# Kernel optimization log

Measured on AMD Instinct MI355X. Metric: run time of the kernel, lower is better.

The kernel has to match this reference:

```python
import jax, jax.numpy as jnp
import numpy as np

C = 16          # number of classes
LAM = 25.0      # lambda_param (invariance)
MU = 25.0       # mu_param (variance)
NU = 1.0        # nu_param (covariance)
ALPHA = 50.0    # alpha_param (class-discriminative margin & weight)
EPS = 1e-4


def setup_inputs() -> dict:
    key = jax.random.key(0)
    k1, k2, k3 = jax.random.split(key, 3)
    N, D = 32768, 256
    z_a = jax.random.normal(k1, (N, D), dtype=jnp.float32)
    z_b = jax.random.normal(k2, (N, D), dtype=jnp.float32)
    labels = jax.random.randint(k3, (N,), 0, C)
    return {"z_a": z_a, "z_b": z_b, "labels": labels}


def _class_stats(x, labels):
    # counts [C], mean [C,D], unbiased var [C,D] via one segmented pass
    ones = jnp.ones(x.shape[0], x.dtype)
    counts = jax.ops.segment_sum(ones, labels, num_segments=C)
    s = jax.ops.segment_sum(x, labels, num_segments=C)
    sq = jax.ops.segment_sum(x * x, labels, num_segments=C)
    mean = s / counts[:, None]
    var = (sq - counts[:, None] * mean * mean) / (counts[:, None] - 1.0)
    return counts, mean, var


def _variance_loss(var):
    # mean over classes of mean_D relu(1 - std); D equal per class -> global mean
    std = jnp.sqrt(var + EPS)
    return jnp.mean(jax.nn.relu(1.0 - std))


def _covariance_loss(x, labels, counts, mean):
    D = x.shape[1]
    e = x - mean[labels]  # centered per class

    def per_class(c):
        w = (labels == c).astype(x.dtype)
        em = e * w[:, None]
        cov = em.T @ em / (counts[c] - 1.0)  # [D, D]
        off = (cov * cov).sum() - (jnp.diagonal(cov) ** 2).sum()
        return off / D

    return jnp.mean(jax.lax.map(per_class, jnp.arange(C)))


def _class_disc_loss(mean_a, mean_b):
    m = 0.5 * (mean_a + mean_b)               # [C, D]
    diff = m[:, None, :] - m[None, :, :]      # [C, C, D]
    d2 = jnp.sum(diff * diff, axis=-1)        # [C, C]
    mask = jnp.triu(jnp.ones((C, C), bool), 1)
    dist = jnp.sqrt(jnp.where(mask, d2, 1.0))  # safe sqrt off-mask
    pen = jnp.where(mask, jax.nn.relu(ALPHA - dist) ** 2, 0.0)
    npairs = C * (C - 1) // 2
    return pen.sum() / npairs


def reference(z_a, z_b, labels):
    inv_loss = jnp.mean((z_a - z_b) ** 2)
    ca, ma, va = _class_stats(z_a, labels)
    cb, mb, vb = _class_stats(z_b, labels)
    var_loss = 0.5 * (_variance_loss(va) + _variance_loss(vb))
    cov_loss = 0.5 * (_covariance_loss(z_a, labels, ca, ma)
                      + _covariance_loss(z_b, labels, cb, mb))
    class_loss = _class_disc_loss(ma, mb)
    return LAM * inv_loss + MU * var_loss + NU * cov_loss + ALPHA * class_loss
```

## Files before the change

kernel.cpp:

```cpp
#include <hip/hip_runtime.h>
#include <math.h>

#define N_ROWS 32768
#define D 256
#define C 16

#define WS_SUMS_A 0
#define WS_SQ_A   4096
#define WS_SUMS_B 8192
#define WS_SQ_B   12288
#define WS_INV    16384
#define WS_COV    16385
#define WS_COUNTS 16392
#define WS_CURSOR 16408
#define WS_POFFP  16424
#define WS_EOFF   16448
#define WS_INVP   16512
#define WS_COVP   17024
#define WS_PERM   17920
#define WS_ZERO_FLOATS 16408

#define WS_PSUM   50688
#define WS_HPART  181760
#define WS_GPART2 189952
#define GP_TILE2P 2048
#define NTASK     10
#define NSPLIT    8
#define KC        2
#define GP_PER_SPLIT2P (NTASK * C * 2 * GP_TILE2P)
#define RIDX_CAP  1024
#define NEED_A ((size_t)(WS_GPART2 + NSPLIT * GP_PER_SPLIT2P) * 4)

typedef __attribute__((ext_vector_type(8))) __bf16 bf16x8;
typedef __attribute__((ext_vector_type(16))) float f32x16;

__device__ inline unsigned bf16_rne(float f) {
    unsigned u = __float_as_uint(f);
    return (u + 0x7fffu + ((u >> 16) & 1u)) >> 16;
}
__device__ inline unsigned pack_bf16(float lo, float hi) {
    return bf16_rne(lo) | (bf16_rne(hi) << 16);
}
__device__ inline int img_base4(int c, int kd) {
    return c * 20 + ((kd + ((c >> 1) & 12)) & 12);
}
__device__ inline int img_base2(int c, int kd) {
    return c * 20 + ((kd + ((c >> 1) & 12)) & 14);
}
__device__ inline void task_rc(int w, int& r, int& c) {
    if (w < 4)      { r = 0; c = w; }
    else if (w < 7) { r = 1; c = w - 3; }
    else if (w < 9) { r = 2; c = w - 5; }
    else            { r = 3; c = 3; }
}


__global__ __launch_bounds__(256) void k_pre(const float* __restrict__ za,
                                             const float* __restrict__ zb,
                                             const int* __restrict__ labels,
                                             int* __restrict__ hpart,
                                             float* __restrict__ ws) {
    const int t = threadIdx.x;
    const int b = blockIdx.x;
    __shared__ int h[C];
    if (t < C) h[t] = 0;
    __syncthreads();
    if (t < 64) atomicAdd(&h[labels[b * 64 + t]], 1);

    const int base = b * 4096 + t;
    float acc = 0.f;
    #pragma unroll
    for (int k = 0; k < 16; ++k) {
        const int i = base + k * 256;
        const float4 a = ((const float4*)za)[i];
        const float4 v = ((const float4*)zb)[i];
        const float dx = a.x - v.x, dy = a.y - v.y;
        const float dz = a.z - v.z, dw = a.w - v.w;
        acc += dx * dx + dy * dy + dz * dz + dw * dw;
    }
    for (int o = 32; o > 0; o >>= 1) acc += __shfl_down(acc, o, 64);
    __shared__ float red[4];
    if ((t & 63) == 0) red[t >> 6] = acc;
    __syncthreads();
    if (t < C) hpart[b * C + t] = h[t];
    if (t == 0) ws[WS_INVP + b] = red[0] + red[1] + red[2] + red[3];
}

__global__ __launch_bounds__(512) void k_scatter2(const int* __restrict__ labels,
                                                  const int* __restrict__ hpart,
                                                  int* __restrict__ counts,
                                                  int* __restrict__ poffp,
                                                  int* __restrict__ eoffp,
                                                  int* __restrict__ perm) {
    const int t = threadIdx.x;
    const int B = blockIdx.x;
    __shared__ int lh[C];
    __shared__ int tot[32][C];
    __shared__ int pre[32][C];
    __shared__ int ccnt[C], cpre[C], ceoff[C];
    const int i = B * 512 + t;
    const int lab = labels[i];
    if (t < C) lh[t] = 0;
    const int c = t & 15, seg = t >> 4;
    {
        int tt = 0, pp = 0;
        const int plo = seg * 16, pcut = B * 8;
        #pragma unroll
        for (int p = plo; p < plo + 16; ++p) {
            const int v = hpart[p * C + c];
            tt += v;
            if (p < pcut) pp += v;
        }
        tot[seg][c] = tt;
        pre[seg][c] = pp;
    }
    __syncthreads();
    const int lr = atomicAdd(&lh[lab], 1);
    if (t < C) {
        int s1 = 0, s2 = 0;
        #pragma unroll
        for (int g = 0; g < 32; ++g) { s1 += tot[g][t]; s2 += pre[g][t]; }
        ccnt[t] = s1;
        cpre[t] = s2;
    }
    __syncthreads();
    if (t == 0) {
        int off = 0, po = 0;
        for (int cc = 0; cc < C; ++cc) {
            ceoff[cc] = off;
            if (B == 0) { eoffp[cc] = off; poffp[cc] = po; counts[cc] = ccnt[cc]; }
            off += ccnt[cc];
            po += (ccnt[cc] + 31) >> 5;
        }
        if (B == 0) { eoffp[C] = off; poffp[C] = po; }
    }
    __syncthreads();
    perm[ceoff[lab] + cpre[lab] + lr] = i;
}

__global__ __launch_bounds__(640) void k_gram6(const float* __restrict__ za,
                                               const float* __restrict__ zb,
                                               const int* __restrict__ perm,
                                               const int* __restrict__ counts,
                                               const int* __restrict__ poffp,
                                               const int* __restrict__ eoffp,
                                               float* __restrict__ ws) {
    const int t = threadIdx.x;
    const int split = blockIdx.x;
    const int cls = blockIdx.y, inp = blockIdx.z;
    const float* X = inp ? zb : za;
    const int cnt = counts[cls];
    const int eoff = eoffp[cls];
    const int nsteps = poffp[cls + 1] - poffp[cls];
    const int chunk = (nsteps + NSPLIT - 1) / NSPLIT;
    const int sb = split * chunk;
    const int se = min(sb + chunk, nsteps);

    __shared__ __align__(16) unsigned img[2][5120];
    __shared__ float sstats[512];
    __shared__ int ridx[RIDX_CAP];

    for (int i = t; i < 512; i += 640) sstats[i] = 0.f;
    const int nl = (se > sb) ? (se - sb) * 32 : 0;
    for (int i = t; i < nl && i < RIDX_CAP; i += 640) {
        const int gr = sb * 32 + i;
        ridx[i] = (gr < cnt) ? perm[eoff + gr] : -1;
    }
    __syncthreads();

    auto rowidx = [&](int li) -> int {
        if (li < RIDX_CAP) return ridx[li];
        const int gr = sb * 32 + li;
        return (gr < cnt) ? perm[eoff + gr] : -1;
    };

    const int lane = t & 63, w = t >> 6;
    const int cg = lane & 31, q = lane >> 5;
    int tr, tc;
    task_rc(w, tr, tc);
    const bool stg = (t < 512);

    const int lc = 4 * (t & 63);
    const int kp0 = 2 * ((t >> 6) & 7);

    f32x16 acc[2][2];
    #pragma unroll
    for (int i = 0; i < 2; ++i)
        #pragma unroll
        for (int j = 0; j < 2; ++j) acc[i][j] = 0.0f;

    float s1r[4] = {0.f, 0.f, 0.f, 0.f};
    float s2r[4] = {0.f, 0.f, 0.f, 0.f};
    float4 f0[2], f1[2];

    auto load_regs = [&](int s) {
        #pragma unroll
        for (int it = 0; it < 2; ++it) {
            const int li = (s - sb) * 32 + 2 * (kp0 + it);
            const int r0 = rowidx(li), r1 = rowidx(li + 1);
            f0[it] = (r0 >= 0) ? *(const float4*)(X + (size_t)r0 * D + lc)
                               : make_float4(0.f, 0.f, 0.f, 0.f);
            f1[it] = (r1 >= 0) ? *(const float4*)(X + (size_t)r1 * D + lc)
                               : make_float4(0.f, 0.f, 0.f, 0.f);
        }
    };
    auto pack_store = [&](int buf) {
        unsigned pw[4][2];
        #pragma unroll
        for (int it = 0; it < 2; ++it) {
            pw[0][it] = pack_bf16(f0[it].x, f1[it].x);
            pw[1][it] = pack_bf16(f0[it].y, f1[it].y);
            pw[2][it] = pack_bf16(f0[it].z, f1[it].z);
            pw[3][it] = pack_bf16(f0[it].w, f1[it].w);
        }
        #pragma unroll
        for (int d = 0; d < 4; ++d)
            *(uint2*)&img[buf][img_base2(lc + d, kp0)] = make_uint2(pw[d][0], pw[d][1]);
        #pragma unroll
        for (int it = 0; it < 2; ++it) {
            s1r[0] += f0[it].x + f1[it].x; s2r[0] += f0[it].x * f0[it].x + f1[it].x * f1[it].x;
            s1r[1] += f0[it].y + f1[it].y; s2r[1] += f0[it].y * f0[it].y + f1[it].y * f1[it].y;
            s1r[2] += f0[it].z + f1[it].z; s2r[2] += f0[it].z * f0[it].z + f1[it].z * f1[it].z;
            s1r[3] += f0[it].w + f1[it].w; s2r[3] += f0[it].w * f0[it].w + f1[it].w * f1[it].w;
        }
    };
    auto frag = [&](int buf, int col, int kd) -> bf16x8 {
        return *(const bf16x8*)&img[buf][img_base4(col, kd)];
    };

    if (sb < se) {
        if (stg) { load_regs(sb); pack_store(0); }
        __syncthreads();
        for (int s = sb; s < se; ++s) {
            const int buf = (s - sb) & 1;
            const bool more = (s + 1 < se);
            if (stg && more) load_regs(s + 1);
            #pragma unroll
            for (int h = 0; h < 2; ++h) {
                const int kd = h * 8 + q * 4;
                bf16x8 a0 = frag(buf, tr * 64 + cg, kd);
                bf16x8 a1 = frag(buf, tr * 64 + 32 + cg, kd);
                bf16x8 b0, b1;
                if (tr == tc) { b0 = a0; b1 = a1; }
                else {
                    b0 = frag(buf, tc * 64 + cg, kd);
                    b1 = frag(buf, tc * 64 + 32 + cg, kd);
                }
                acc[0][0] = __builtin_amdgcn_mfma_f32_32x32x16_bf16(a0, b0, acc[0][0], 0, 0, 0);
                acc[0][1] = __builtin_amdgcn_mfma_f32_32x32x16_bf16(a0, b1, acc[0][1], 0, 0, 0);
                acc[1][0] = __builtin_amdgcn_mfma_f32_32x32x16_bf16(a1, b0, acc[1][0], 0, 0, 0);
                acc[1][1] = __builtin_amdgcn_mfma_f32_32x32x16_bf16(a1, b1, acc[1][1], 0, 0, 0);
            }
            if (stg && more) pack_store(buf ^ 1);
            __syncthreads();
        }
    }

    unsigned* gp = (unsigned*)ws + WS_GPART2 + (size_t)split * GP_PER_SPLIT2P
                 + (((size_t)cls * 2 + inp) * NTASK + w) * GP_TILE2P;
    #pragma unroll
    for (int i = 0; i < 2; ++i)
        #pragma unroll
        for (int r = 0; r < 16; ++r) {
            const int row = i * 32 + (r & 3) + 8 * (r >> 2) + 4 * q;
            gp[row * 32 + cg] = pack_bf16(acc[i][0][r], acc[i][1][r]);
        }

    if (stg) {
        #pragma unroll
        for (int d = 0; d < 4; ++d) {
            atomicAdd(&sstats[lc + d],       s1r[d]);
            atomicAdd(&sstats[256 + lc + d], s2r[d]);
        }
    }
    __syncthreads();
    const size_t pbase = (((size_t)split * C + cls) * 2 + inp) * 512;
    for (int i = t; i < 512; i += 640) ws[WS_PSUM + pbase + i] = sstats[i];
}

__global__ __launch_bounds__(256) void k_cov4(const int* __restrict__ counts,
                                              float* __restrict__ ws) {
    const int t = threadIdx.x;
    const int w = blockIdx.x / KC, k0 = blockIdx.x % KC;
    int tr, tc;
    task_rc(w, tr, tc);
    const int cls = blockIdx.y, inp = blockIdx.z;
    const int cnt = counts[cls];
    const float fc = (float)cnt;
    const float cinv = 1.f / fc, uinv = 1.f / (fc - 1.f);
    const float wgt = (tr == tc) ? 1.f : 2.f;
    __shared__ float Mr[64], Mc[64];
    if (t < 64) {
        float s = 0.f;
        #pragma unroll
        for (int sp = 0; sp < NSPLIT; ++sp)
            s += ws[WS_PSUM + (((size_t)sp * C + cls) * 2 + inp) * 512 + tr * 64 + t];
        Mr[t] = s * cinv;
    } else if (t < 128) {
        const int u = t - 64;
        float s = 0.f;
        #pragma unroll
        for (int sp = 0; sp < NSPLIT; ++sp)
            s += ws[WS_PSUM + (((size_t)sp * C + cls) * 2 + inp) * 512 + tc * 64 + u];
        Mc[u] = s * cinv;
    }
    if (w == 0 && k0 == 0) {
        float s1 = 0.f, s2 = 0.f;
        #pragma unroll
        for (int sp = 0; sp < NSPLIT; ++sp) {
            const size_t pb = WS_PSUM + (((size_t)sp * C + cls) * 2 + inp) * 512;
            s1 += ws[pb + t];
            s2 += ws[pb + 256 + t];
        }
        ws[(inp ? WS_SUMS_B : WS_SUMS_A) + cls * D + t] = s1;
        ws[(inp ? WS_SQ_B   : WS_SQ_A)   + cls * D + t] = s2;
    }
    __syncthreads();

    const int e0 = k0 * 1024 + t * 4;
    const unsigned* gp0 = (const unsigned*)ws + WS_GPART2
                        + (((size_t)cls * 2 + inp) * NTASK + w) * GP_TILE2P + e0;
    uint4 u4[NSPLIT];
    #pragma unroll
    for (int sp = 0; sp < NSPLIT; ++sp)
        u4[sp] = *(const uint4*)(gp0 + (size_t)sp * GP_PER_SPLIT2P);

    float glo[4] = {0.f, 0.f, 0.f, 0.f};
    float ghi[4] = {0.f, 0.f, 0.f, 0.f};
    #pragma unroll
    for (int sp = 0; sp < NSPLIT; ++sp) {
        const unsigned* uu = (const unsigned*)&u4[sp];
        #pragma unroll
        for (int j = 0; j < 4; ++j) {
            glo[j] += __uint_as_float(uu[j] << 16);
            ghi[j] += __uint_as_float(uu[j] & 0xffff0000u);
        }
    }
    const int row = e0 >> 5, c0 = e0 & 31;
    const float mr = Mr[row];
    float local = 0.f;
    #pragma unroll
    for (int j = 0; j < 4; ++j) {
        const float clo = (glo[j] - fc * mr * Mc[c0 + j]) * uinv;
        const float chi = (ghi[j] - fc * mr * Mc[c0 + j + 32]) * uinv;
        if (!(tr == tc && row == c0 + j))      local += wgt * clo * clo;
        if (!(tr == tc && row == c0 + j + 32)) local += wgt * chi * chi;
    }
    for (int o = 32; o > 0; o >>= 1) local += __shfl_down(local, o, 64);
    __shared__ float red[4];
    if ((t & 63) == 0) red[t >> 6] = local;
    __syncthreads();
    if (t == 0)
        ws[WS_COVP + (((size_t)inp * C + cls) * NTASK + w) * KC + k0] =
            red[0] + red[1] + red[2] + red[3];
}

__global__ __launch_bounds__(512) void k_hist(const int* __restrict__ labels,
                                              int* __restrict__ counts) {
    __shared__ int h[C];
    const int t = threadIdx.x;
    if (t < C) h[t] = 0;
    __syncthreads();
    const int i = blockIdx.x * 512 + t;
    atomicAdd(&h[labels[i]], 1);
    __syncthreads();
    if (t < C) atomicAdd(&counts[t], h[t]);
}

__global__ void k_scan(const int* __restrict__ counts, int* __restrict__ cursor,
                       int* __restrict__ poffp, int* __restrict__ eoffp) {
    if (threadIdx.x == 0) {
        int off = 0, po = 0;
        for (int c = 0; c < C; ++c) {
            cursor[c] = off;
            eoffp[c] = off;
            poffp[c] = po;
            off += counts[c];
            po += (counts[c] + 31) >> 5;
        }
        poffp[C] = po;
        eoffp[C] = off;
    }
}

__global__ __launch_bounds__(512) void k_scatter(const int* __restrict__ labels,
                                                 int* __restrict__ cursor,
                                                 int* __restrict__ perm) {
    __shared__ int lh[C];
    __shared__ int lbase[C];
    const int t = threadIdx.x;
    if (t < C) lh[t] = 0;
    __syncthreads();
    const int i = blockIdx.x * 512 + t;
    const int lab = labels[i];
    const int lr = atomicAdd(&lh[lab], 1);
    __syncthreads();
    if (t < C) lbase[t] = atomicAdd(&cursor[t], lh[t]);
    __syncthreads();
    perm[lbase[lab] + lr] = i;
}

__global__ __launch_bounds__(256) void k_stats(const float* __restrict__ za,
                                               const float* __restrict__ zb,
                                               const int* __restrict__ labels,
                                               float* __restrict__ ws) {
    const int t = threadIdx.x;
    __shared__ float S[4][C * D];
    __shared__ int lab[512];
    for (int i = t; i < 4 * C * D; i += 256) ((float*)S)[i] = 0.f;
    const int r0 = blockIdx.x * 512;
    for (int i = t; i < 512; i += 256) lab[i] = labels[r0 + i];
    __syncthreads();
    float invp = 0.f;
    #pragma unroll 4
    for (int rr = 0; rr < 512; ++rr) {
        const int l = lab[rr];
        const float a = za[(size_t)(r0 + rr) * D + t];
        const float b = zb[(size_t)(r0 + rr) * D + t];
        const float dd = a - b;
        invp += dd * dd;
        S[0][l * D + t] += a;
        S[1][l * D + t] += a * a;
        S[2][l * D + t] += b;
        S[3][l * D + t] += b * b;
    }
    __syncthreads();
    #pragma unroll
    for (int c = 0; c < C; ++c) {
        atomicAdd(&ws[WS_SUMS_A + c * D + t], S[0][c * D + t]);
        atomicAdd(&ws[WS_SQ_A   + c * D + t], S[1][c * D + t]);
        atomicAdd(&ws[WS_SUMS_B + c * D + t], S[2][c * D + t]);
        atomicAdd(&ws[WS_SQ_B   + c * D + t], S[3][c * D + t]);
    }
    for (int o = 32; o > 0; o >>= 1) invp += __shfl_down(invp, o, 64);
    if ((t & 63) == 0) atomicAdd(&ws[WS_INV], invp);
}

#define STR 20
#define KB 32
__global__ __launch_bounds__(256) void k_gram_slow(const float* __restrict__ za,
                                                   const float* __restrict__ zb,
                                                   const int* __restrict__ perm,
                                                   const int* __restrict__ counts,
                                                   float* __restrict__ ws) {
    const int t = threadIdx.x;
    const int tile = blockIdx.x;
    const int tx = tile >> 1, ty = (tile + 1) >> 1;
    const int cls = blockIdx.y;
    const int inp = blockIdx.z;
    const float* X = inp ? zb : za;
    const float* sums = ws + (inp ? WS_SUMS_B : WS_SUMS_A) + cls * D;
    int offs = 0;
    for (int c = 0; c < cls; ++c) offs += counts[c];
    const int cnt = counts[cls];
    const int cm0 = tx * 128, cn0 = ty * 128;
    __shared__ __align__(16) unsigned lds[2][256 * STR];
    const int p = t >> 5, cq = t & 31;
    const int lane = t & 63, w = t >> 6;
    const int wr = w & 1, wc = w >> 1;
    const int cg = lane & 31, q = lane >> 5;
    f32x16 acc[2][2];
    #pragma unroll
    for (int i = 0; i < 2; ++i)
        #pragma unroll
        for (int j = 0; j < 2; ++j) acc[i][j] = 0.0f;
    const int nsteps = (cnt + KB - 1) / KB;
    auto stage = [&](int buf, int k0) {
        #pragma unroll
        for (int ch = 0; ch < 2; ++ch) {
            const int gc = (ch ? cn0 : cm0) + 4 * cq;
            #pragma unroll
            for (int sub = 0; sub < 2; ++sub) {
                const int rr = sub * 16 + 2 * p;
                const int r0 = k0 + rr, r1 = r0 + 1;
                float4 v0 = make_float4(0.f, 0.f, 0.f, 0.f), v1 = v0;
                if (r0 < cnt) v0 = *(const float4*)(X + (size_t)perm[offs + r0] * D + gc);
                if (r1 < cnt) v1 = *(const float4*)(X + (size_t)perm[offs + r1] * D + gc);
                unsigned* dst = &lds[buf][(ch * 128 + 4 * cq) * STR + (rr >> 1)];
                dst[0 * STR] = pack_bf16(v0.x, v1.x);
                dst[1 * STR] = pack_bf16(v0.y, v1.y);
                dst[2 * STR] = pack_bf16(v0.z, v1.z);
                dst[3 * STR] = pack_bf16(v0.w, v1.w);
            }
        }
    };
    auto frag = [&](int buf, int colbase, int h) -> bf16x8 {
        return *(const bf16x8*)&lds[buf][(colbase + cg) * STR + h * 8 + q * 4];
    };
    stage(0, 0);
    for (int s = 0; s < nsteps; ++s) {
        __syncthreads();
        const int buf = s & 1;
        if (s + 1 < nsteps) stage(buf ^ 1, (s + 1) * KB);
        #pragma unroll
        for (int h = 0; h < 2; ++h) {
            bf16x8 a0 = frag(buf, wr * 64, h);
            bf16x8 a1 = frag(buf, wr * 64 + 32, h);
            bf16x8 b0 = frag(buf, 128 + wc * 64, h);
            bf16x8 b1 = frag(buf, 128 + wc * 64 + 32, h);
            acc[0][0] = __builtin_amdgcn_mfma_f32_32x32x16_bf16(a0, b0, acc[0][0], 0, 0, 0);
            acc[0][1] = __builtin_amdgcn_mfma_f32_32x32x16_bf16(a0, b1, acc[0][1], 0, 0, 0);
            acc[1][0] = __builtin_amdgcn_mfma_f32_32x32x16_bf16(a1, b0, acc[1][0], 0, 0, 0);
            acc[1][1] = __builtin_amdgcn_mfma_f32_32x32x16_bf16(a1, b1, acc[1][1], 0, 0, 0);
        }
    }
    const float fc = (float)cnt;
    const float cinv = 1.f / fc, uinv = 1.f / (fc - 1.f);
    const float wgt = (tx == ty) ? 1.f : 2.f;
    float local = 0.f;
    #pragma unroll
    for (int i = 0; i < 2; ++i) {
        #pragma unroll
        for (int j = 0; j < 2; ++j) {
            const int gn = cn0 + wc * 64 + j * 32 + (lane & 31);
            const float mn = sums[gn] * cinv;
            #pragma unroll
            for (int r = 0; r < 16; ++r) {
                const int row = (r & 3) + 8 * (r >> 2) + 4 * q;
                const int gm = cm0 + wr * 64 + i * 32 + row;
                const float cov = (acc[i][j][r] - fc * (sums[gm] * cinv) * mn) * uinv;
                if (gm != gn) local += wgt * cov * cov;
            }
        }
    }
    for (int o = 32; o > 0; o >>= 1) local += __shfl_down(local, o, 64);
    if (lane == 0) atomicAdd(&ws[WS_COV], local);
}

__global__ __launch_bounds__(256) void k_final(const float* __restrict__ ws,
                                               float* __restrict__ out,
                                               int fast) {
    __shared__ float M[C * D];
    __shared__ float redv[4], redi[4], redc[4], redp[4];
    const int t = threadIdx.x;
    const int* counts = (const int*)ws + WS_COUNTS;

    float vsum = 0.f;
    for (int idx = t; idx < 2 * C * D; idx += 256) {
        const int inp = idx >> 12;
        const int cd = idx & 4095;
        const int c = cd >> 8;
        const float cnt = (float)counts[c];
        const float s  = ws[(inp ? WS_SUMS_B : WS_SUMS_A) + cd];
        const float sq = ws[(inp ? WS_SQ_B   : WS_SQ_A)   + cd];
        const float mean = s / cnt;
        const float var = (sq - cnt * mean * mean) / (cnt - 1.f);
        vsum += fmaxf(1.f - sqrtf(var + 1e-4f), 0.f);
    }
    float isum, csum;
    if (fast) {
        isum = ws[WS_INVP + t] + ws[WS_INVP + 256 + t];
        csum = ws[WS_COVP + t] + ws[WS_COVP + 256 + t]
             + ((t < 128) ? ws[WS_COVP + 512 + t] : 0.f);
    } else {
        isum = (t == 0) ? ws[WS_INV] : 0.f;
        csum = (t == 0) ? ws[WS_COV] : 0.f;
    }
    for (int cd = t; cd < C * D; cd += 256) {
        const int c = cd >> 8;
        const float cnt = (float)counts[c];
        M[cd] = 0.5f * (ws[WS_SUMS_A + cd] + ws[WS_SUMS_B + cd]) / cnt;
    }
    for (int o = 32; o > 0; o >>= 1) {
        vsum += __shfl_down(vsum, o, 64);
        isum += __shfl_down(isum, o, 64);
        csum += __shfl_down(csum, o, 64);
    }
    if ((t & 63) == 0) {
        redv[t >> 6] = vsum; redi[t >> 6] = isum; redc[t >> 6] = csum;
    }
    __syncthreads();

    const int wv = t >> 6, ln = t & 63;
    float psum = 0.f;
    int p = 0;
    for (int i = 0; i < C; ++i) {
        for (int j = i + 1; j < C; ++j, ++p) {
            if ((p & 3) != wv) continue;
            float d2 = 0.f;
            #pragma unroll
            for (int d = ln; d < D; d += 64) {
                const float df = M[i * D + d] - M[j * D + d];
                d2 += df * df;
            }
            for (int o = 32; o > 0; o >>= 1) d2 += __shfl_down(d2, o, 64);
            if (ln == 0) {
                const float dist = sqrtf(d2);
                const float r = fmaxf(50.f - dist, 0.f);
                psum += r * r;
            }
        }
    }
    if (ln == 0) redp[wv] = psum;
    __syncthreads();

    if (t == 0) {
        const float var_loss = (redv[0] + redv[1] + redv[2] + redv[3]) / 8192.f;
        const float class_loss = (redp[0] + redp[1] + redp[2] + redp[3]) / 120.f;
        const float inv_loss = (redi[0] + redi[1] + redi[2] + redi[3]) / (float)(N_ROWS * D);
        const float cov_loss = 0.5f * (redc[0] + redc[1] + redc[2] + redc[3]) / (float)(C * D);
        out[0] = 25.f * inv_loss + 25.f * var_loss + 1.f * cov_loss + 50.f * class_loss;
    }
}

extern "C" void kernel_launch(void* const* d_in, const int* in_sizes, int n_in,
                              void* d_out, int out_size, void* d_ws, size_t ws_size,
                              hipStream_t stream) {
    const float* za = (const float*)d_in[0];
    const float* zb = (const float*)d_in[1];
    const int* labels = (const int*)d_in[2];
    float* out = (float*)d_out;
    float* ws = (float*)d_ws;
    int* wsi = (int*)d_ws;

    if (ws_size >= NEED_A) {
        k_pre<<<512, 256, 0, stream>>>(za, zb, labels, wsi + WS_HPART, ws);
        k_scatter2<<<64, 512, 0, stream>>>(labels, wsi + WS_HPART, wsi + WS_COUNTS,
                                           wsi + WS_POFFP, wsi + WS_EOFF, wsi + WS_PERM);
        k_gram6<<<dim3(NSPLIT, C, 2), 640, 0, stream>>>(
            za, zb, wsi + WS_PERM, wsi + WS_COUNTS, wsi + WS_POFFP,
            wsi + WS_EOFF, ws);
        k_cov4<<<dim3(NTASK * KC, C, 2), 256, 0, stream>>>(wsi + WS_COUNTS, ws);
        k_final<<<1, 256, 0, stream>>>(ws, out, 1);
    } else {
        hipMemsetAsync(d_ws, 0, WS_ZERO_FLOATS * sizeof(float), stream);
        k_hist<<<64, 512, 0, stream>>>(labels, wsi + WS_COUNTS);
        k_scan<<<1, 64, 0, stream>>>(wsi + WS_COUNTS, wsi + WS_CURSOR,
                                     wsi + WS_POFFP, wsi + WS_EOFF);
        k_scatter<<<64, 512, 0, stream>>>(labels, wsi + WS_CURSOR, wsi + WS_PERM);
        k_stats<<<64, 256, 0, stream>>>(za, zb, labels, ws);
        k_gram_slow<<<dim3(3, C, 2), 256, 0, stream>>>(za, zb, wsi + WS_PERM,
                                                       wsi + WS_COUNTS, ws);
        k_final<<<1, 256, 0, stream>>>(ws, out, 0);
    }
}
```

Baseline: 159.5 us.

## Fuse invariance loss into gram kernel and slim the histogram pre-pass

The separate pre-pass kernel read all of z_a and z_b only to compute the squared-difference sum. That work now happens inside the gram kernel: blocks for input A also load the matching z_b rows and accumulate the invariance term, writing one partial per split and class. The pre-pass shrinks to a label histogram over 64 blocks, and the scatter prefix logic is changed to match. This drops one full read of both inputs, but it doubles the global loads in the input-A gram blocks and so unbalances the work between inputs A and B.

```diff
diff --git a/kernel.cpp b/kernel.cpp
--- a/kernel.cpp
+++ b/kernel.cpp
@@ -55,35 +55,15 @@
 }
 
 
-__global__ __launch_bounds__(256) void k_pre(const float* __restrict__ za,
-                                             const float* __restrict__ zb,
-                                             const int* __restrict__ labels,
-                                             int* __restrict__ hpart,
-                                             float* __restrict__ ws) {
-    const int t = threadIdx.x;
-    const int b = blockIdx.x;
+__global__ __launch_bounds__(512) void k_hist2(const int* __restrict__ labels,
+                                               int* __restrict__ hpart) {
     __shared__ int h[C];
+    const int t = threadIdx.x;
     if (t < C) h[t] = 0;
     __syncthreads();
-    if (t < 64) atomicAdd(&h[labels[b * 64 + t]], 1);
-
-    const int base = b * 4096 + t;
-    float acc = 0.f;
-    #pragma unroll
-    for (int k = 0; k < 16; ++k) {
-        const int i = base + k * 256;
-        const float4 a = ((const float4*)za)[i];
-        const float4 v = ((const float4*)zb)[i];
-        const float dx = a.x - v.x, dy = a.y - v.y;
-        const float dz = a.z - v.z, dw = a.w - v.w;
-        acc += dx * dx + dy * dy + dz * dz + dw * dw;
-    }
-    for (int o = 32; o > 0; o >>= 1) acc += __shfl_down(acc, o, 64);
-    __shared__ float red[4];
-    if ((t & 63) == 0) red[t >> 6] = acc;
-    __syncthreads();
-    if (t < C) hpart[b * C + t] = h[t];
-    if (t == 0) ws[WS_INVP + b] = red[0] + red[1] + red[2] + red[3];
+    atomicAdd(&h[labels[blockIdx.x * 512 + t]], 1);
+    __syncthreads();
+    if (t < C) hpart[blockIdx.x * C + t] = h[t];
 }
 
 __global__ __launch_bounds__(512) void k_scatter2(const int* __restrict__ labels,
@@ -103,16 +83,10 @@
     if (t < C) lh[t] = 0;
     const int c = t & 15, seg = t >> 4;
     {
-        int tt = 0, pp = 0;
-        const int plo = seg * 16, pcut = B * 8;
-        #pragma unroll
-        for (int p = plo; p < plo + 16; ++p) {
-            const int v = hpart[p * C + c];
-            tt += v;
-            if (p < pcut) pp += v;
-        }
-        tot[seg][c] = tt;
-        pre[seg][c] = pp;
+        const int p0 = 2 * seg, p1 = p0 + 1;
+        const int v0 = hpart[p0 * C + c], v1 = hpart[p1 * C + c];
+        tot[seg][c] = v0 + v1;
+        pre[seg][c] = (p0 < B ? v0 : 0) + (p1 < B ? v1 : 0);
     }
     __syncthreads();
     const int lr = atomicAdd(&lh[lab], 1);
@@ -138,7 +112,7 @@
     perm[ceoff[lab] + cpre[lab] + lr] = i;
 }
 
-__global__ __launch_bounds__(640) void k_gram6(const float* __restrict__ za,
+__global__ __launch_bounds__(640) void k_gram7(const float* __restrict__ za,
                                                const float* __restrict__ zb,
                                                const int* __restrict__ perm,
                                                const int* __restrict__ counts,
@@ -158,6 +132,7 @@
 
     __shared__ __align__(16) unsigned img[2][5120];
     __shared__ float sstats[512];
+    __shared__ float redI[8];
     __shared__ int ridx[RIDX_CAP];
 
     for (int i = t; i < 512; i += 640) sstats[i] = 0.f;
@@ -191,7 +166,9 @@
 
     float s1r[4] = {0.f, 0.f, 0.f, 0.f};
     float s2r[4] = {0.f, 0.f, 0.f, 0.f};
+    float accI = 0.f;
     float4 f0[2], f1[2];
+    float4 g0[2], g1[2];
 
     auto load_regs = [&](int s) {
         #pragma unroll
@@ -202,6 +179,12 @@
                                : make_float4(0.f, 0.f, 0.f, 0.f);
             f1[it] = (r1 >= 0) ? *(const float4*)(X + (size_t)r1 * D + lc)
                                : make_float4(0.f, 0.f, 0.f, 0.f);
+            if (inp == 0) {
+                g0[it] = (r0 >= 0) ? *(const float4*)(zb + (size_t)r0 * D + lc)
+                                   : make_float4(0.f, 0.f, 0.f, 0.f);
+                g1[it] = (r1 >= 0) ? *(const float4*)(zb + (size_t)r1 * D + lc)
+                                   : make_float4(0.f, 0.f, 0.f, 0.f);
+            }
         }
     };
     auto pack_store = [&](int buf) {
@@ -222,6 +205,16 @@
             s1r[1] += f0[it].y + f1[it].y; s2r[1] += f0[it].y * f0[it].y + f1[it].y * f1[it].y;
             s1r[2] += f0[it].z + f1[it].z; s2r[2] += f0[it].z * f0[it].z + f1[it].z * f1[it].z;
             s1r[3] += f0[it].w + f1[it].w; s2r[3] += f0[it].w * f0[it].w + f1[it].w * f1[it].w;
+        }
+        if (inp == 0) {
+            #pragma unroll
+            for (int it = 0; it < 2; ++it) {
+                float d0, d1;
+                d0 = f0[it].x - g0[it].x; d1 = f1[it].x - g1[it].x; accI += d0 * d0 + d1 * d1;
+                d0 = f0[it].y - g0[it].y; d1 = f1[it].y - g1[it].y; accI += d0 * d0 + d1 * d1;
+                d0 = f0[it].z - g0[it].z; d1 = f1[it].z - g1[it].z; accI += d0 * d0 + d1 * d1;
+                d0 = f0[it].w - g0[it].w; d1 = f1[it].w - g1[it].w; accI += d0 * d0 + d1 * d1;
+            }
         }
     };
     auto frag = [&](int buf, int col, int kd) -> bf16x8 {
@@ -266,6 +259,11 @@
             gp[row * 32 + cg] = pack_bf16(acc[i][0][r], acc[i][1][r]);
         }
 
+    if (inp == 0 && stg) {
+        float v = accI;
+        for (int o = 32; o > 0; o >>= 1) v += __shfl_down(v, o, 64);
+        if (lane == 0) redI[w] = v;
+    }
     if (stg) {
         #pragma unroll
         for (int d = 0; d < 4; ++d) {
@@ -274,6 +272,12 @@
         }
     }
     __syncthreads();
+    if (inp == 0 && t == 0) {
+        float s = 0.f;
+        #pragma unroll
+        for (int k = 0; k < 8; ++k) s += redI[k];
+        ws[WS_INVP + split * C + cls] = s;
+    }
     const size_t pbase = (((size_t)split * C + cls) * 2 + inp) * 512;
     for (int i = t; i < 512; i += 640) ws[WS_PSUM + pbase + i] = sstats[i];
 }
@@ -549,7 +553,7 @@
     }
     float isum, csum;
     if (fast) {
-        isum = ws[WS_INVP + t] + ws[WS_INVP + 256 + t];
+        isum = (t < 128) ? ws[WS_INVP + t] : 0.f;
         csum = ws[WS_COVP + t] + ws[WS_COVP + 256 + t]
              + ((t < 128) ? ws[WS_COVP + 512 + t] : 0.f);
     } else {
@@ -614,10 +618,10 @@
     int* wsi = (int*)d_ws;
 
     if (ws_size >= NEED_A) {
-        k_pre<<<512, 256, 0, stream>>>(za, zb, labels, wsi + WS_HPART, ws);
+        k_hist2<<<64, 512, 0, stream>>>(labels, wsi + WS_HPART);
         k_scatter2<<<64, 512, 0, stream>>>(labels, wsi + WS_HPART, wsi + WS_COUNTS,
                                            wsi + WS_POFFP, wsi + WS_EOFF, wsi + WS_PERM);
-        k_gram6<<<dim3(NSPLIT, C, 2), 640, 0, stream>>>(
+        k_gram7<<<dim3(NSPLIT, C, 2), 640, 0, stream>>>(
             za, zb, wsi + WS_PERM, wsi + WS_COUNTS, wsi + WS_POFFP,
             wsi + WS_EOFF, ws);
         k_cov4<<<dim3(NTASK * KC, C, 2), 256, 0, stream>>>(wsi + WS_COUNTS, ws);
```

New measurement: 159.1 us. Within noise of the previous version (-0.2%).
